# Kernel tuning notes

Measured on AMD Instinct MI355X. Metric: run time of the kernel, lower is better.

Reference implementation:

```python
import jax, jax.numpy as jnp
import numpy as np
import itertools, math

# Static config (matches init_kwargs)
DIM = 384
KEY_DIM = 16
NUM_HEADS = 8
ATTN_RATIO = 4
RES = 14
OUT_DIM = 768
RES2 = math.ceil(RES / 2)          # 7
N = RES * RES                      # 196
N2 = RES2 * RES2                   # 49
D = ATTN_RATIO * KEY_DIM           # 64
NH_KD = NUM_HEADS * KEY_DIM        # 128
DH = NUM_HEADS * D                 # 512
SCALE = KEY_DIM ** -0.5
BATCH = 512


def _build_bias_idxs():
    points = list(itertools.product(range(RES), range(RES)))
    points_ = list(itertools.product(range(RES2), range(RES2)))
    ratio = math.ceil(RES / RES2)
    offsets = {}
    idxs = []
    for p1 in points_:
        for p2 in points:
            off = (abs(p1[0] * ratio - p2[0]), abs(p1[1] * ratio - p2[1]))
            if off not in offsets:
                offsets[off] = len(offsets)
            idxs.append(offsets[off])
    return np.array(idxs, dtype=np.int32).reshape(N2, N), len(offsets)


def setup_inputs() -> dict:
    key = jax.random.key(0)
    ks = jax.random.split(key, 16)
    idxs_np, n_off = _build_bias_idxs()
    w = lambda k, shape, s=0.05: (jax.random.normal(k, shape, jnp.float32) * s)
    inp = {
        "x": jax.random.normal(ks[0], (BATCH, DIM, RES, RES), jnp.float32),
        # LGQuery: depthwise 3x3 s2 conv (groups=DIM), then 1x1 conv + BN (folded scale/shift)
        "q_local_w": w(ks[1], (DIM, 1, 3, 3)),
        "q_local_b": w(ks[2], (DIM,)),
        "q_proj_w": w(ks[3], (NH_KD, DIM)),
        "q_proj_b": w(ks[4], (NH_KD,)),
        "q_bn_s": 1.0 + w(ks[5], (NH_KD,)),
        "q_bn_t": w(ks[5], (NH_KD,)),
        # k: 1x1 conv + BN
        "k_w": w(ks[6], (NH_KD, DIM)),
        "k_b": w(ks[7], (NH_KD,)),
        "k_bn_s": 1.0 + w(ks[8], (NH_KD,)),
        "k_bn_t": w(ks[8], (NH_KD,)),
        # v: 1x1 conv + BN
        "v_w": w(ks[9], (DH, DIM)),
        "v_b": w(ks[10], (DH,)),
        "v_bn_s": 1.0 + w(ks[10], (DH,)),
        "v_bn_t": w(ks[10], (DH,)),
        # v_local: depthwise 3x3 s2 (groups=DH) + BN
        "vl_w": w(ks[11], (DH, 1, 3, 3)),
        "vl_b": w(ks[12], (DH,)),
        "vl_bn_s": 1.0 + w(ks[12], (DH,)),
        "vl_bn_t": w(ks[12], (DH,)),
        # proj: GELU -> 1x1 conv -> BN
        "p_w": w(ks[13], (OUT_DIM, DH)),
        "p_b": w(ks[14], (OUT_DIM,)),
        "p_bn_s": 1.0 + w(ks[14], (OUT_DIM,)),
        "p_bn_t": w(ks[14], (OUT_DIM,)),
        # learned relative-position biases + gather indices
        "attn_biases": w(ks[15], (NUM_HEADS, n_off), 0.02),
        "bias_idxs": jnp.asarray(idxs_np),  # [N2, N] int32
    }
    return inp


def _dwconv_s2(x, w, b):
    # depthwise 3x3, stride 2, pad 1, NCHW
    C = x.shape[1]
    y = jax.lax.conv_general_dilated(
        x, w, window_strides=(2, 2), padding=((1, 1), (1, 1)),
        feature_group_count=C, dimension_numbers=("NCHW", "OIHW", "NCHW"))
    return y + b[None, :, None, None]


def _conv1x1_bn(x, w, b, s, t):
    y = jnp.einsum("bchw,oc->bohw", x, w) + b[None, :, None, None]
    return y * s[None, :, None, None] + t[None, :, None, None]


def reference(x, q_local_w, q_local_b, q_proj_w, q_proj_b, q_bn_s, q_bn_t,
              k_w, k_b, k_bn_s, k_bn_t, v_w, v_b, v_bn_s, v_bn_t,
              vl_w, vl_b, vl_bn_s, vl_bn_t, p_w, p_b, p_bn_s, p_bn_t,
              attn_biases, bias_idxs):
    B = x.shape[0]
    # LGQuery: depthwise conv + avgpool(k=1,s=2)==stride subsample, then 1x1+BN
    ql = _dwconv_s2(x, q_local_w, q_local_b) + x[:, :, ::2, ::2]
    q = _conv1x1_bn(ql, q_proj_w, q_proj_b, q_bn_s, q_bn_t)        # [B,128,7,7]
    q = q.reshape(B, NUM_HEADS, KEY_DIM, N2).transpose(0, 1, 3, 2)  # bhqc

    k = _conv1x1_bn(x, k_w, k_b, k_bn_s, k_bn_t).reshape(B, NUM_HEADS, KEY_DIM, N)  # bhck

    v4 = _conv1x1_bn(x, v_w, v_b, v_bn_s, v_bn_t)                   # [B,512,14,14]
    v_local = _dwconv_s2(v4, vl_w, vl_b)
    v_local = v_local * vl_bn_s[None, :, None, None] + vl_bn_t[None, :, None, None]
    v = v4.reshape(B, NUM_HEADS, D, N).transpose(0, 1, 3, 2)        # bhkd

    bias = attn_biases[:, bias_idxs]                                # [H,N2,N]
    attn = jax.nn.softmax(jnp.einsum("bhqc,bhck->bhqk", q, k) * SCALE + bias[None], axis=-1)
    out = jnp.einsum("bhqk,bhkd->bhqd", attn, v)                    # [B,H,N2,D]
    out = out.transpose(0, 1, 3, 2).reshape(B, DH, RES2, RES2) + v_local
    out = jax.nn.gelu(out, approximate=False)                       # torch nn.GELU default (erf)
    out = _conv1x1_bn(out, p_w, p_b, p_bn_s, p_bn_t)                # [B,768,7,7]
    return out
```

## Files before the change

kernel.cpp:

```cpp
#include <hip/hip_runtime.h>
#include <math.h>

#define DIM 384
#define NUM_HEADS 8
#define RES 14
#define RES2 7
#define NPOS 196
#define N2 49
#define DHEAD 64
#define NH_KD 128
#define DH 512
#define OUT_DIM 768
#define BATCH 512
#define SCALE_Q 0.25f

typedef unsigned short u16;
typedef short s16x8 __attribute__((ext_vector_type(8)));
typedef short s16x4 __attribute__((ext_vector_type(4)));
typedef float f32x4 __attribute__((ext_vector_type(4)));
typedef unsigned int u32x2 __attribute__((ext_vector_type(2)));

__device__ __forceinline__ float bf2f(u16 u) {
  union { unsigned int i; float f; } v; v.i = ((unsigned int)u) << 16; return v.f;
}
__device__ __forceinline__ u16 f2bf(float f) {
  union { unsigned int i; float f; } v; v.f = f;
  unsigned int r = v.i + 0x7fffu + ((v.i >> 16) & 1u);
  return (u16)(r >> 16);
}

#define GLD16(gp, lp) __builtin_amdgcn_global_load_lds( \
    (const __attribute__((address_space(1))) void*)(gp), \
    (__attribute__((address_space(3))) void*)(lp), 16, 0, 0)

__global__ __launch_bounds__(256) void k_prep(const float* __restrict__ kw, const float* __restrict__ vw,
                                              const float* __restrict__ qw, const float* __restrict__ pw,
                                              const float* __restrict__ ab, const int* __restrict__ idxs, int noff,
                                              const float* __restrict__ kb, const float* __restrict__ kbs, const float* __restrict__ kbt,
                                              const float* __restrict__ vb, const float* __restrict__ vbs, const float* __restrict__ vbt,
                                              u16* __restrict__ wb, u16* __restrict__ qwb, u16* __restrict__ pwb,
                                              float* __restrict__ bxp,
                                              float* __restrict__ cvb, float* __restrict__ cvs, float* __restrict__ cvt) {
  int i = blockIdx.x * 256 + threadIdx.x;
  const int E1 = 640 * DIM;
  const int E2 = E1 + NH_KD * DIM;
  const int E3 = E2 + OUT_DIM * DH;
  const int E4 = E3 + NUM_HEADS * N2 * 256;
  const int E5 = E4 + 3 * 640;
  if (i < E1) wb[i] = f2bf(i < DH * DIM ? vw[i] : kw[i - DH * DIM]);
  else if (i < E2) qwb[i - E1] = f2bf(qw[i - E1]);
  else if (i < E3) pwb[i - E2] = f2bf(pw[i - E2]);
  else if (i < E4) {
    int j = i - E3;
    int f = j & 15, c = (j >> 4) & 15;
    int m = (j >> 8) % N2, h = j / (N2 * 256);
    int n = f * 16 + c;
    bxp[j] = (n < NPOS) ? ab[h * noff + idxs[m * NPOS + n]] : 0.f;
  } else if (i < E5) {
    int j = i - E4; int c = j % 640, t = j / 640;
    float v = (c < DH) ? (t == 0 ? vb[c] : t == 1 ? vbs[c] : vbt[c])
                       : (t == 0 ? kb[c - DH] : t == 1 ? kbs[c - DH] : kbt[c - DH]);
    (t == 0 ? cvb : t == 1 ? cvs : cvt)[c] = v;
  }
}

__global__ __launch_bounds__(256) void k_transpose(const float* __restrict__ x, u16* __restrict__ xt) {
  int b = blockIdx.y, c0 = blockIdx.x * 64;
  __shared__ u16 tile[64][196];
  int tid = threadIdx.x, wave = tid >> 6, lane = tid & 63;
  const float* xb = x + (size_t)b * DIM * NPOS;
  for (int r = wave; r < 64; r += 4) {
    const float* row = xb + (size_t)(c0 + r) * NPOS;
    tile[r][lane]       = f2bf(row[lane]);
    tile[r][lane + 64]  = f2bf(row[lane + 64]);
    tile[r][lane + 128] = f2bf(row[lane + 128]);
    if (lane < 4) tile[r][lane + 192] = f2bf(row[lane + 192]);
  }
  __syncthreads();
  u16* xtb = xt + (size_t)b * NPOS * DIM;
  for (int n = wave; n < NPOS; n += 4)
    xtb[(size_t)n * DIM + c0 + lane] = tile[lane][n];
}

__global__ __launch_bounds__(256) void k_dwconv_q8(const u16* __restrict__ xt, const float* __restrict__ w,
                                                   const float* __restrict__ bias, u16* __restrict__ qlt) {
  int b = blockIdx.y;
  int lid = blockIdx.x * 256 + threadIdx.x;
  if (lid >= N2 * (DIM / 8)) return;
  int n2 = lid / (DIM / 8), c0 = (lid % (DIM / 8)) * 8;
  int r = n2 / RES2, s = n2 % RES2;
  const u16* xb = xt + (size_t)b * NPOS * DIM + c0;

  s16x8 xv[9];
#pragma unroll
  for (int dy = 0; dy < 3; dy++) {
    int ry = 2 * r - 1 + dy;
#pragma unroll
    for (int dx = 0; dx < 3; dx++) {
      int sx = 2 * s - 1 + dx;
      if (ry >= 0 && ry < RES && sx >= 0 && sx < RES)
        xv[dy * 3 + dx] = *(const s16x8*)(xb + (size_t)(ry * RES + sx) * DIM);
      else
        xv[dy * 3 + dx] = (s16x8){0, 0, 0, 0, 0, 0, 0, 0};
    }
  }
  s16x8 resid = *(const s16x8*)(xb + (size_t)(2 * r * RES + 2 * s) * DIM);
  s16x8 o;
#pragma unroll
  for (int e = 0; e < 8; e++) {
    const float* we = w + (size_t)(c0 + e) * 9;
    float a = bias[c0 + e] + bf2f((u16)resid[e]);
#pragma unroll
    for (int t = 0; t < 9; t++) a += we[t] * bf2f((u16)xv[t][e]);
    o[e] = (short)f2bf(a);
  }
  *(s16x8*)(qlt + ((size_t)b * N2 + n2) * DIM + c0) = o;
}

template <int SPLN, bool F32OUT, bool KMERGE>
__global__ __launch_bounds__(256) void k_gemm_flat(
    const u16* __restrict__ A, const u16* __restrict__ B, void* __restrict__ C, void* __restrict__ C2,
    const float* __restrict__ cb, const float* __restrict__ bns, const float* __restrict__ bnt,
    int K, int NMT, int ldc, long bstride) {
  __shared__ __align__(16) u16 a_lds[2 * 128 * 32];
  __shared__ __align__(16) u16 b_lds[2 * 128 * 32];
  int nwg = gridDim.x, bx = blockIdx.x;
  int wg = ((nwg & 7) == 0) ? ((bx & 7) * (nwg >> 3) + (bx >> 3)) : bx;
  int mt = wg % NMT, nt = wg / NMT;
  int m0 = mt * 128, n0 = nt * 128;
  int tid = threadIdx.x, w = tid >> 6, l = tid & 63;

  int srow = l >> 2;
  int scol = ((l & 3) ^ ((l >> 3) & 3)) * 8;
  const u16* asrc[2]; const u16* bsrc[2];
#pragma unroll
  for (int c = 0; c < 2; c++) {
    int chunk = w * 2 + c;
    asrc[c] = A + (size_t)(m0 + chunk * 16 + srow) * K + scol;
    bsrc[c] = B + (size_t)(n0 + chunk * 16 + srow) * K + scol;
  }
  char* adst = (char*)a_lds + (w * 2) * 1024 + l * 16;
  char* bdst = (char*)b_lds + (w * 2) * 1024 + l * 16;

  f32x4 acc[4][4];
#pragma unroll
  for (int i = 0; i < 4; i++)
#pragma unroll
    for (int j = 0; j < 4; j++) acc[i][j] = (f32x4){0.f, 0.f, 0.f, 0.f};

  int wm = w >> 1, wn = w & 1;
  int rg8 = ((l >> 4) ^ ((l >> 1) & 3)) * 8;
  int arow = wm * 64 + (l & 15);
  int brow = wn * 64 + (l & 15);

  for (int kk = 0; kk < K; kk += 64) {
#pragma unroll
    for (int c = 0; c < 2; c++) {
      GLD16(asrc[c] + kk,      adst + c * 1024);
      GLD16(asrc[c] + kk + 32, adst + 8192 + c * 1024);
      GLD16(bsrc[c] + kk,      bdst + c * 1024);
      GLD16(bsrc[c] + kk + 32, bdst + 8192 + c * 1024);
    }
    __syncthreads();
#pragma unroll
    for (int hf = 0; hf < 2; hf++) {
      const u16* ah = a_lds + hf * (128 * 32);
      const u16* bh = b_lds + hf * (128 * 32);
      s16x8 af[4], bf[4];
#pragma unroll
      for (int i = 0; i < 4; i++) {
        af[i] = *(const s16x8*)(&ah[(arow + i * 16) * 32 + rg8]);
        bf[i] = *(const s16x8*)(&bh[(brow + i * 16) * 32 + rg8]);
      }
#pragma unroll
      for (int i = 0; i < 4; i++)
#pragma unroll
        for (int j = 0; j < 4; j++)
          acc[i][j] = __builtin_amdgcn_mfma_f32_16x16x32_bf16(af[i], bf[j], acc[i][j], 0, 0, 0);
    }
    __syncthreads();
  }

  int ncol = l & 15, mq = (l >> 4) * 4;
#pragma unroll
  for (int i = 0; i < 4; i++) {
#pragma unroll
    for (int j = 0; j < 4; j++) {
      int n = n0 + wn * 64 + j * 16 + ncol;
#pragma unroll
      for (int r = 0; r < 4; r++) {
        int m = m0 + wm * 64 + i * 16 + mq + r;
        int ch = (SPLN || KMERGE) ? m : n;
        float val = acc[i][j][r] * bns[ch] + (cb[ch] * bns[ch] + bnt[ch]);
        if (KMERGE && m0 >= DH) {
          ((u16*)C2)[(size_t)n * NH_KD + (m - DH)] = f2bf(val);
        } else {
          size_t o;
          if (SPLN) o = (size_t)(n / SPLN) * bstride + (size_t)m * SPLN + (n % SPLN);
          else      o = (size_t)m * ldc + n;
          if (F32OUT) ((float*)C)[o] = val;
          else        ((u16*)C)[o] = f2bf(val);
        }
      }
    }
  }
}

__global__ __launch_bounds__(256) void k_dwconv_v(const u16* __restrict__ v4, const float* __restrict__ w,
    const float* __restrict__ bias, const float* __restrict__ bns, const float* __restrict__ bnt,
    u16* __restrict__ vlt) {
  int b = blockIdx.y, ct = blockIdx.x;
  __shared__ u16 tile[64][196];
  int tid = threadIdx.x, wave = tid >> 6, lane = tid & 63;
  const u16* vbp = v4 + ((size_t)b * DH + ct * 64) * NPOS;
  for (int r = wave; r < 64; r += 4) {
    const u16* row = vbp + (size_t)r * NPOS;
    tile[r][lane]       = row[lane];
    tile[r][lane + 64]  = row[lane + 64];
    tile[r][lane + 128] = row[lane + 128];
    if (lane < 4) tile[r][lane + 192] = row[lane + 192];
  }
  __syncthreads();
  for (int idx = tid; idx < 64 * N2; idx += 256) {
    int cl = idx & 63, n2 = idx >> 6;
    int ch = ct * 64 + cl;
    int r = n2 / RES2, s = n2 % RES2;
    float acc = bias[ch];
#pragma unroll
    for (int dy = 0; dy < 3; dy++) {
      int ry = 2 * r - 1 + dy;
      if (ry < 0 || ry >= RES) continue;
#pragma unroll
      for (int dx = 0; dx < 3; dx++) {
        int sx = 2 * s - 1 + dx;
        if (sx < 0 || sx >= RES) continue;
        acc += w[ch * 9 + dy * 3 + dx] * bf2f(tile[cl][ry * RES + sx]);
      }
    }
    vlt[((size_t)b * N2 + n2) * DH + ch] = f2bf(acc * bns[ch] + bnt[ch]);
  }
}

__global__ __launch_bounds__(256, 4) void k_attn_mfma(const u16* __restrict__ qT, const u16* __restrict__ kT,
    const u16* __restrict__ v4, const float* __restrict__ bxp, const u16* __restrict__ vlT,
    u16* __restrict__ gT) {
  int h = blockIdx.x, b = blockIdx.y;
  __shared__ __align__(16) u16 p_lds[64 * 232];
  float* o_lds = (float*)p_lds;
  int tid = threadIdx.x, w = tid >> 6, l = tid & 63;
  int part = l >> 4, row16 = l & 15;
  int mbase = w * 16 + part * 4;
  int ncol = l & 15;

  for (int idx = tid; idx < 64 * 8; idx += 256)
    ((uint*)&p_lds[(idx >> 3) * 232])[104 + (idx & 7)] = 0;

  s16x8 af = (s16x8){0, 0, 0, 0, 0, 0, 0, 0};
  if (part < 2)
    af = *(const s16x8*)(qT + ((size_t)b * N2 + (w * 16 + row16)) * NH_KD + h * 16 + part * 8);

  const u16* kbase = kT + (size_t)b * NPOS * NH_KD + h * 16 + part * 8;
  f32x4 s[13];
#pragma unroll
  for (int f = 0; f < 13; f++) {
    s16x8 bf = (s16x8){0, 0, 0, 0, 0, 0, 0, 0};
    if (part < 2)
      bf = *(const s16x8*)(kbase + (size_t)(f * 16 + row16) * NH_KD);
    s[f] = __builtin_amdgcn_mfma_f32_16x16x32_bf16(af, bf, (f32x4){0.f, 0.f, 0.f, 0.f}, 0, 0, 0);
  }

  const u16* vbase = v4 + ((size_t)b * DH + h * DHEAD) * NPOS;
  int vd = l & 15, vq8 = part * 8;
  auto VLOAD = [&](int f, int kk) {
    const u16* p = vbase + (size_t)(f * 16 + vd) * NPOS + kk + vq8;
    s16x8 r;
    ((u32x2*)&r)[0] = *(const u32x2*)(p);
    ((u32x2*)&r)[1] = *(const u32x2*)(p + 4);
    return r;
  };
  s16x8 vb0[4];
#pragma unroll
  for (int f = 0; f < 4; f++) vb0[f] = VLOAD(f, 0);

#pragma unroll
  for (int q = 0; q < 4; q++) {
    f32x4 bqr[4];
#pragma unroll
    for (int r = 0; r < 4; r++) {
      int mm = mbase + r; if (mm > N2 - 1) mm = N2 - 1;
      bqr[r] = *(const f32x4*)(bxp + (((size_t)h * N2 + mm) * 16 + ncol) * 16 + q * 4);
    }
#pragma unroll
    for (int ff = 0; ff < 4; ff++) {
      int f = q * 4 + ff;
      if (f < 13) {
        int n = f * 16 + ncol;
#pragma unroll
        for (int r = 0; r < 4; r++) {
          int m = mbase + r;
          s[f][r] = (m < N2 && n < NPOS) ? s[f][r] * SCALE_Q + bqr[r][ff] : -1e30f;
        }
      }
    }
  }
#pragma unroll
  for (int r = 0; r < 4; r++) {
    float mx = s[0][r];
#pragma unroll
    for (int f = 1; f < 13; f++) mx = fmaxf(mx, s[f][r]);
    mx = fmaxf(mx, __shfl_xor(mx, 1)); mx = fmaxf(mx, __shfl_xor(mx, 2));
    mx = fmaxf(mx, __shfl_xor(mx, 4)); mx = fmaxf(mx, __shfl_xor(mx, 8));
    float sum = 0.f;
#pragma unroll
    for (int f = 0; f < 13; f++) { s[f][r] = __expf(s[f][r] - mx); sum += s[f][r]; }
    sum += __shfl_xor(sum, 1); sum += __shfl_xor(sum, 2);
    sum += __shfl_xor(sum, 4); sum += __shfl_xor(sum, 8);
    float inv = 1.f / sum;
#pragma unroll
    for (int f = 0; f < 13; f++) s[f][r] *= inv;
  }
#pragma unroll
  for (int f = 0; f < 13; f++) {
    int n = f * 16 + ncol;
#pragma unroll
    for (int r = 0; r < 4; r++)
      p_lds[(mbase + r) * 232 + n] = f2bf(s[f][r]);
  }
  __syncthreads();

  f32x4 o[4];
#pragma unroll
  for (int f = 0; f < 4; f++) o[f] = (f32x4){0.f, 0.f, 0.f, 0.f};
#pragma unroll
  for (int t = 0; t < 7; t++) {
    int kk = t * 32;
    s16x8 vn[4];
    if (t < 6) {
#pragma unroll
      for (int f = 0; f < 4; f++) vn[f] = VLOAD(f, kk + 32);
    }
    s16x8 pa = *(const s16x8*)(&p_lds[(w * 16 + row16) * 232 + kk + part * 8]);
#pragma unroll
    for (int f = 0; f < 4; f++)
      o[f] = __builtin_amdgcn_mfma_f32_16x16x32_bf16(pa, vb0[f], o[f], 0, 0, 0);
    if (t < 6) {
#pragma unroll
      for (int f = 0; f < 4; f++) vb0[f] = vn[f];
    }
  }
  __syncthreads();

#pragma unroll
  for (int f = 0; f < 4; f++)
#pragma unroll
    for (int r = 0; r < 4; r++) {
      int m = mbase + r;
      if (m < N2) o_lds[m * 68 + f * 16 + ncol] = o[f][r];
    }
  __syncthreads();

  for (int idx = tid; idx < N2 * 16; idx += 256) {
    int row = idx >> 4, c4 = (idx & 15) << 2;
    f32x4 ov = *(const f32x4*)(&o_lds[row * 68 + c4]);
    size_t go = ((size_t)b * N2 + row) * DH + h * DHEAD + c4;
    s16x4 vv = *(const s16x4*)(vlT + go);
    s16x4 outv;
#pragma unroll
    for (int e = 0; e < 4; e++) {
      float xv = ov[e] + bf2f((u16)vv[e]);
      float g = 0.5f * xv * (1.f + erff(xv * 0.70710678118f));
      outv[e] = (short)f2bf(g);
    }
    *(s16x4*)(gT + go) = outv;
  }
}

extern "C" void kernel_launch(void* const* d_in, const int* in_sizes, int n_in,
                              void* d_out, int out_size, void* d_ws, size_t ws_size,
                              hipStream_t stream) {
  const float* x   = (const float*)d_in[0];
  const float* qlw = (const float*)d_in[1];
  const float* qlb = (const float*)d_in[2];
  const float* qpw = (const float*)d_in[3];
  const float* qpb = (const float*)d_in[4];
  const float* qbs = (const float*)d_in[5];
  const float* qbt = (const float*)d_in[6];
  const float* kw  = (const float*)d_in[7];
  const float* kb  = (const float*)d_in[8];
  const float* kbs = (const float*)d_in[9];
  const float* kbt = (const float*)d_in[10];
  const float* vw  = (const float*)d_in[11];
  const float* vb  = (const float*)d_in[12];
  const float* vbs = (const float*)d_in[13];
  const float* vbt = (const float*)d_in[14];
  const float* vlw = (const float*)d_in[15];
  const float* vlb = (const float*)d_in[16];
  const float* vls = (const float*)d_in[17];
  const float* vlt_in = (const float*)d_in[18];
  const float* pw  = (const float*)d_in[19];
  const float* pb  = (const float*)d_in[20];
  const float* pbs = (const float*)d_in[21];
  const float* pbt = (const float*)d_in[22];
  const float* ab  = (const float*)d_in[23];
  const int*   bidx = (const int*)d_in[24];
  int noff = in_sizes[23] / NUM_HEADS;

  char* ws = (char*)d_ws;
  size_t off = 0;
  auto alloc = [&](size_t bytes) { char* p = ws + off; off += (bytes + 255) & ~(size_t)255; return p; };
  u16* xbT = (u16*)alloc((size_t)BATCH * NPOS * DIM * 2);
  u16* kTm = (u16*)alloc((size_t)BATCH * NPOS * NH_KD * 2);
  u16* qlT = (u16*)alloc((size_t)BATCH * N2 * DIM * 2);
  u16* qTm = (u16*)alloc((size_t)BATCH * N2 * NH_KD * 2);
  u16* v4m = (u16*)alloc((size_t)BATCH * DH * NPOS * 2);
  u16* vlTm = (u16*)alloc((size_t)BATCH * N2 * DH * 2);
  float* bxp = (float*)alloc((size_t)NUM_HEADS * N2 * 16 * 16 * 4);
  u16* wb  = (u16*)alloc((size_t)640 * DIM * 2);
  u16* qwb = (u16*)alloc((size_t)NH_KD * DIM * 2);
  u16* pwb = (u16*)alloc((size_t)OUT_DIM * DH * 2);
  float* cvb = (float*)alloc(640 * 4);
  float* cvs = (float*)alloc(640 * 4);
  float* cvt = (float*)alloc(640 * 4);
  u16* gTm = xbT;

  k_prep<<<(890752 + 255) / 256, 256, 0, stream>>>(kw, vw, qpw, pw, ab, bidx, noff,
                                                   kb, kbs, kbt, vb, vbs, vbt,
                                                   wb, qwb, pwb, bxp, cvb, cvs, cvt);

  k_transpose<<<dim3(6, BATCH), 256, 0, stream>>>(x, xbT);
  k_dwconv_q8<<<dim3((N2 * (DIM / 8) + 255) / 256, BATCH), 256, 0, stream>>>(xbT, qlw, qlb, qlT);

  k_gemm_flat<NPOS, false, true><<<3920, 256, 0, stream>>>(
      wb, xbT, v4m, kTm, cvb, cvs, cvt, DIM, 5, 0, (long)DH * NPOS);
  k_gemm_flat<0, false, false><<<196, 256, 0, stream>>>(
      qlT, qwb, qTm, nullptr, qpb, qbs, qbt, DIM, 196, NH_KD, 0);

  k_dwconv_v<<<dim3(8, BATCH), 256, 0, stream>>>(v4m, vlw, vlb, vls, vlt_in, vlTm);
  k_attn_mfma<<<dim3(NUM_HEADS, BATCH), 256, 0, stream>>>(qTm, kTm, v4m, bxp, vlTm, gTm);

  k_gemm_flat<N2, true, false><<<1176, 256, 0, stream>>>(
      pwb, gTm, d_out, nullptr, pb, pbs, pbt, DH, 6, 0, (long)OUT_DIM * N2);
}
```

Before: 418.4 us.

## Fuse q depthwise conv into transpose and merge V/K/Q projection GEMMs

Computes the q-branch depthwise 3x3 stride-2 conv directly from the LDS tile in the transpose kernel, removing a separate kernel that re-read the transposed activations from global memory. The V, K and Q 1x1-conv GEMMs now run in one launch, with block-index ranges choosing the operands. K is computed in transposed orientation (activations as A, weights as B), so its output is written row-contiguous instead of via the scattered KMERGE path. This cuts launches and makes the small Q GEMM run alongside the large one, at the cost of per-block branching and scalar conv work inside the transpose kernel.

```diff
diff --git a/kernel.cpp b/kernel.cpp
--- a/kernel.cpp
+++ b/kernel.cpp
@@ -36,37 +36,35 @@
 __global__ __launch_bounds__(256) void k_prep(const float* __restrict__ kw, const float* __restrict__ vw,
                                               const float* __restrict__ qw, const float* __restrict__ pw,
                                               const float* __restrict__ ab, const int* __restrict__ idxs, int noff,
-                                              const float* __restrict__ kb, const float* __restrict__ kbs, const float* __restrict__ kbt,
-                                              const float* __restrict__ vb, const float* __restrict__ vbs, const float* __restrict__ vbt,
-                                              u16* __restrict__ wb, u16* __restrict__ qwb, u16* __restrict__ pwb,
-                                              float* __restrict__ bxp,
-                                              float* __restrict__ cvb, float* __restrict__ cvs, float* __restrict__ cvt) {
+                                              u16* __restrict__ kwb, u16* __restrict__ vwb,
+                                              u16* __restrict__ qwb, u16* __restrict__ pwb,
+                                              float* __restrict__ bxp) {
   int i = blockIdx.x * 256 + threadIdx.x;
-  const int E1 = 640 * DIM;
-  const int E2 = E1 + NH_KD * DIM;
-  const int E3 = E2 + OUT_DIM * DH;
-  const int E4 = E3 + NUM_HEADS * N2 * 256;
-  const int E5 = E4 + 3 * 640;
-  if (i < E1) wb[i] = f2bf(i < DH * DIM ? vw[i] : kw[i - DH * DIM]);
-  else if (i < E2) qwb[i - E1] = f2bf(qw[i - E1]);
-  else if (i < E3) pwb[i - E2] = f2bf(pw[i - E2]);
-  else if (i < E4) {
-    int j = i - E3;
+  const int e1 = NH_KD * DIM;
+  const int e2 = e1 + DH * DIM;
+  const int e3 = e2 + NH_KD * DIM;
+  const int e4 = e3 + OUT_DIM * DH;
+  const int e5 = e4 + NUM_HEADS * N2 * 256;
+  if (i < e1) kwb[i] = f2bf(kw[i]);
+  else if (i < e2) vwb[i - e1] = f2bf(vw[i - e1]);
+  else if (i < e3) qwb[i - e2] = f2bf(qw[i - e2]);
+  else if (i < e4) pwb[i - e3] = f2bf(pw[i - e3]);
+  else if (i < e5) {
+    int j = i - e4;
     int f = j & 15, c = (j >> 4) & 15;
     int m = (j >> 8) % N2, h = j / (N2 * 256);
     int n = f * 16 + c;
     bxp[j] = (n < NPOS) ? ab[h * noff + idxs[m * NPOS + n]] : 0.f;
-  } else if (i < E5) {
-    int j = i - E4; int c = j % 640, t = j / 640;
-    float v = (c < DH) ? (t == 0 ? vb[c] : t == 1 ? vbs[c] : vbt[c])
-                       : (t == 0 ? kb[c - DH] : t == 1 ? kbs[c - DH] : kbt[c - DH]);
-    (t == 0 ? cvb : t == 1 ? cvs : cvt)[c] = v;
-  }
-}
-
-__global__ __launch_bounds__(256) void k_transpose(const float* __restrict__ x, u16* __restrict__ xt) {
+  }
+}
+
+__global__ __launch_bounds__(256) void k_transpose_dwq(const float* __restrict__ x, u16* __restrict__ xt,
+                                                       const float* __restrict__ qlw, const float* __restrict__ qlb,
+                                                       u16* __restrict__ qlt) {
   int b = blockIdx.y, c0 = blockIdx.x * 64;
   __shared__ u16 tile[64][196];
+  __shared__ float wlds[576];
+  __shared__ float blds[64];
   int tid = threadIdx.x, wave = tid >> 6, lane = tid & 63;
   const float* xb = x + (size_t)b * DIM * NPOS;
   for (int r = wave; r < 64; r += 4) {
@@ -76,50 +74,126 @@
     tile[r][lane + 128] = f2bf(row[lane + 128]);
     if (lane < 4) tile[r][lane + 192] = f2bf(row[lane + 192]);
   }
+  for (int i = tid; i < 576; i += 256) wlds[i] = qlw[c0 * 9 + i];
+  if (tid < 64) blds[tid] = qlb[c0 + tid];
   __syncthreads();
   u16* xtb = xt + (size_t)b * NPOS * DIM;
   for (int n = wave; n < NPOS; n += 4)
     xtb[(size_t)n * DIM + c0 + lane] = tile[lane][n];
-}
-
-__global__ __launch_bounds__(256) void k_dwconv_q8(const u16* __restrict__ xt, const float* __restrict__ w,
-                                                   const float* __restrict__ bias, u16* __restrict__ qlt) {
-  int b = blockIdx.y;
-  int lid = blockIdx.x * 256 + threadIdx.x;
-  if (lid >= N2 * (DIM / 8)) return;
-  int n2 = lid / (DIM / 8), c0 = (lid % (DIM / 8)) * 8;
-  int r = n2 / RES2, s = n2 % RES2;
-  const u16* xb = xt + (size_t)b * NPOS * DIM + c0;
-
-  s16x8 xv[9];
-#pragma unroll
-  for (int dy = 0; dy < 3; dy++) {
-    int ry = 2 * r - 1 + dy;
-#pragma unroll
-    for (int dx = 0; dx < 3; dx++) {
-      int sx = 2 * s - 1 + dx;
-      if (ry >= 0 && ry < RES && sx >= 0 && sx < RES)
-        xv[dy * 3 + dx] = *(const s16x8*)(xb + (size_t)(ry * RES + sx) * DIM);
-      else
-        xv[dy * 3 + dx] = (s16x8){0, 0, 0, 0, 0, 0, 0, 0};
-    }
-  }
-  s16x8 resid = *(const s16x8*)(xb + (size_t)(2 * r * RES + 2 * s) * DIM);
-  s16x8 o;
-#pragma unroll
-  for (int e = 0; e < 8; e++) {
-    const float* we = w + (size_t)(c0 + e) * 9;
-    float a = bias[c0 + e] + bf2f((u16)resid[e]);
-#pragma unroll
-    for (int t = 0; t < 9; t++) a += we[t] * bf2f((u16)xv[t][e]);
-    o[e] = (short)f2bf(a);
-  }
-  *(s16x8*)(qlt + ((size_t)b * N2 + n2) * DIM + c0) = o;
-}
-
-template <int SPLN, bool F32OUT, bool KMERGE>
+  for (int idx = tid; idx < 64 * N2; idx += 256) {
+    int cl = idx & 63, n2 = idx >> 6;
+    int r = n2 / RES2, s = n2 % RES2;
+    float acc = blds[cl] + bf2f(tile[cl][(2 * r) * RES + 2 * s]);
+#pragma unroll
+    for (int dy = 0; dy < 3; dy++) {
+      int ry = 2 * r - 1 + dy;
+      if (ry < 0 || ry >= RES) continue;
+#pragma unroll
+      for (int dx = 0; dx < 3; dx++) {
+        int sx = 2 * s - 1 + dx;
+        if (sx < 0 || sx >= RES) continue;
+        acc += wlds[cl * 9 + dy * 3 + dx] * bf2f(tile[cl][ry * RES + sx]);
+      }
+    }
+    qlt[((size_t)b * N2 + n2) * DIM + c0 + cl] = f2bf(acc);
+  }
+}
+
+__global__ __launch_bounds__(256) void k_gemm3(
+    const u16* __restrict__ xbT, const u16* __restrict__ qlT,
+    const u16* __restrict__ vwb, const u16* __restrict__ kwb, const u16* __restrict__ qwb,
+    u16* __restrict__ v4m, u16* __restrict__ kTm, u16* __restrict__ qTm,
+    const float* __restrict__ vb, const float* __restrict__ vbs, const float* __restrict__ vbt,
+    const float* __restrict__ kb, const float* __restrict__ kbs, const float* __restrict__ kbt,
+    const float* __restrict__ qpb, const float* __restrict__ qbs, const float* __restrict__ qbt) {
+  __shared__ __align__(16) u16 a_lds[2 * 128 * 32];
+  __shared__ __align__(16) u16 b_lds[2 * 128 * 32];
+  int bx = blockIdx.x;
+  const u16 *A, *B; u16* C;
+  const float *cb, *bns, *bnt;
+  int NMT, ldc, mode, lnwg, lbx;
+  if (bx < 3136)      { A = vwb; B = xbT; C = v4m; cb = vb;  bns = vbs; bnt = vbt; NMT = 4;   ldc = 0;     mode = 1; lnwg = 3136; lbx = bx; }
+  else if (bx < 3920) { A = xbT; B = kwb; C = kTm; cb = kb;  bns = kbs; bnt = kbt; NMT = 784; ldc = NH_KD; mode = 0; lnwg = 784;  lbx = bx - 3136; }
+  else                { A = qlT; B = qwb; C = qTm; cb = qpb; bns = qbs; bnt = qbt; NMT = 196; ldc = NH_KD; mode = 0; lnwg = 196;  lbx = bx - 3920; }
+  int wg = ((lnwg & 7) == 0) ? ((lbx & 7) * (lnwg >> 3) + (lbx >> 3)) : lbx;
+  int mt = wg % NMT, nt = wg / NMT;
+  int m0 = mt * 128, n0 = nt * 128;
+  int tid = threadIdx.x, w = tid >> 6, l = tid & 63;
+
+  int srow = l >> 2;
+  int scol = ((l & 3) ^ ((l >> 3) & 3)) * 8;
+  const u16* asrc[2]; const u16* bsrc[2];
+#pragma unroll
+  for (int c = 0; c < 2; c++) {
+    int chunk = w * 2 + c;
+    asrc[c] = A + (size_t)(m0 + chunk * 16 + srow) * DIM + scol;
+    bsrc[c] = B + (size_t)(n0 + chunk * 16 + srow) * DIM + scol;
+  }
+  char* adst = (char*)a_lds + (w * 2) * 1024 + l * 16;
+  char* bdst = (char*)b_lds + (w * 2) * 1024 + l * 16;
+
+  f32x4 acc[4][4];
+#pragma unroll
+  for (int i = 0; i < 4; i++)
+#pragma unroll
+    for (int j = 0; j < 4; j++) acc[i][j] = (f32x4){0.f, 0.f, 0.f, 0.f};
+
+  int wm = w >> 1, wn = w & 1;
+  int rg8 = ((l >> 4) ^ ((l >> 1) & 3)) * 8;
+  int arow = wm * 64 + (l & 15);
+  int brow = wn * 64 + (l & 15);
+
+  for (int kk = 0; kk < DIM; kk += 64) {
+#pragma unroll
+    for (int c = 0; c < 2; c++) {
+      GLD16(asrc[c] + kk,      adst + c * 1024);
+      GLD16(asrc[c] + kk + 32, adst + 8192 + c * 1024);
+      GLD16(bsrc[c] + kk,      bdst + c * 1024);
+      GLD16(bsrc[c] + kk + 32, bdst + 8192 + c * 1024);
+    }
+    __syncthreads();
+#pragma unroll
+    for (int hf = 0; hf < 2; hf++) {
+      const u16* ah = a_lds + hf * (128 * 32);
+      const u16* bh = b_lds + hf * (128 * 32);
+      s16x8 af[4], bf[4];
+#pragma unroll
+      for (int i = 0; i < 4; i++) {
+        af[i] = *(const s16x8*)(&ah[(arow + i * 16) * 32 + rg8]);
+        bf[i] = *(const s16x8*)(&bh[(brow + i * 16) * 32 + rg8]);
+      }
+#pragma unroll
+      for (int i = 0; i < 4; i++)
+#pragma unroll
+        for (int j = 0; j < 4; j++)
+          acc[i][j] = __builtin_amdgcn_mfma_f32_16x16x32_bf16(af[i], bf[j], acc[i][j], 0, 0, 0);
+    }
+    __syncthreads();
+  }
+
+  int ncol = l & 15, mq = (l >> 4) * 4;
+#pragma unroll
+  for (int i = 0; i < 4; i++) {
+#pragma unroll
+    for (int j = 0; j < 4; j++) {
+      int n = n0 + wn * 64 + j * 16 + ncol;
+#pragma unroll
+      for (int r = 0; r < 4; r++) {
+        int m = m0 + wm * 64 + i * 16 + mq + r;
+        int ch = mode ? m : n;
+        float val = acc[i][j][r] * bns[ch] + (cb[ch] * bns[ch] + bnt[ch]);
+        size_t o;
+        if (mode) o = (size_t)(n / NPOS) * ((long)DH * NPOS) + (size_t)m * NPOS + (n % NPOS);
+        else      o = (size_t)m * ldc + n;
+        C[o] = f2bf(val);
+      }
+    }
+  }
+}
+
+template <int SPLN, bool F32OUT>
 __global__ __launch_bounds__(256) void k_gemm_flat(
-    const u16* __restrict__ A, const u16* __restrict__ B, void* __restrict__ C, void* __restrict__ C2,
+    const u16* __restrict__ A, const u16* __restrict__ B, void* __restrict__ C,
     const float* __restrict__ cb, const float* __restrict__ bns, const float* __restrict__ bnt,
     int K, int NMT, int ldc, long bstride) {
   __shared__ __align__(16) u16 a_lds[2 * 128 * 32];
@@ -190,17 +264,13 @@
 #pragma unroll
       for (int r = 0; r < 4; r++) {
         int m = m0 + wm * 64 + i * 16 + mq + r;
-        int ch = (SPLN || KMERGE) ? m : n;
+        int ch = SPLN ? m : n;
         float val = acc[i][j][r] * bns[ch] + (cb[ch] * bns[ch] + bnt[ch]);
-        if (KMERGE && m0 >= DH) {
-          ((u16*)C2)[(size_t)n * NH_KD + (m - DH)] = f2bf(val);
-        } else {
-          size_t o;
-          if (SPLN) o = (size_t)(n / SPLN) * bstride + (size_t)m * SPLN + (n % SPLN);
-          else      o = (size_t)m * ldc + n;
-          if (F32OUT) ((float*)C)[o] = val;
-          else        ((u16*)C)[o] = f2bf(val);
-        }
+        size_t o;
+        if (SPLN) o = (size_t)(n / SPLN) * bstride + (size_t)m * SPLN + (n % SPLN);
+        else      o = (size_t)m * ldc + n;
+        if (F32OUT) ((float*)C)[o] = val;
+        else        ((u16*)C)[o] = f2bf(val);
       }
     }
   }
@@ -415,29 +485,23 @@
   u16* v4m = (u16*)alloc((size_t)BATCH * DH * NPOS * 2);
   u16* vlTm = (u16*)alloc((size_t)BATCH * N2 * DH * 2);
   float* bxp = (float*)alloc((size_t)NUM_HEADS * N2 * 16 * 16 * 4);
-  u16* wb  = (u16*)alloc((size_t)640 * DIM * 2);
+  u16* kwb = (u16*)alloc((size_t)NH_KD * DIM * 2);
+  u16* vwb = (u16*)alloc((size_t)DH * DIM * 2);
   u16* qwb = (u16*)alloc((size_t)NH_KD * DIM * 2);
   u16* pwb = (u16*)alloc((size_t)OUT_DIM * DH * 2);
-  float* cvb = (float*)alloc(640 * 4);
-  float* cvs = (float*)alloc(640 * 4);
-  float* cvt = (float*)alloc(640 * 4);
   u16* gTm = xbT;
 
-  k_prep<<<(890752 + 255) / 256, 256, 0, stream>>>(kw, vw, qpw, pw, ab, bidx, noff,
-                                                   kb, kbs, kbt, vb, vbs, vbt,
-                                                   wb, qwb, pwb, bxp, cvb, cvs, cvt);
-
-  k_transpose<<<dim3(6, BATCH), 256, 0, stream>>>(x, xbT);
-  k_dwconv_q8<<<dim3((N2 * (DIM / 8) + 255) / 256, BATCH), 256, 0, stream>>>(xbT, qlw, qlb, qlT);
-
-  k_gemm_flat<NPOS, false, true><<<3920, 256, 0, stream>>>(
-      wb, xbT, v4m, kTm, cvb, cvs, cvt, DIM, 5, 0, (long)DH * NPOS);
-  k_gemm_flat<0, false, false><<<196, 256, 0, stream>>>(
-      qlT, qwb, qTm, nullptr, qpb, qbs, qbt, DIM, 196, NH_KD, 0);
+  k_prep<<<(788480 + 255) / 256, 256, 0, stream>>>(kw, vw, qpw, pw, ab, bidx, noff,
+                                                   kwb, vwb, qwb, pwb, bxp);
+
+  k_transpose_dwq<<<dim3(6, BATCH), 256, 0, stream>>>(x, xbT, qlw, qlb, qlT);
+
+  k_gemm3<<<4116, 256, 0, stream>>>(xbT, qlT, vwb, kwb, qwb, v4m, kTm, qTm,
+                                    vb, vbs, vbt, kb, kbs, kbt, qpb, qbs, qbt);
 
   k_dwconv_v<<<dim3(8, BATCH), 256, 0, stream>>>(v4m, vlw, vlb, vls, vlt_in, vlTm);
   k_attn_mfma<<<dim3(NUM_HEADS, BATCH), 256, 0, stream>>>(qTm, kTm, v4m, bxp, vlTm, gTm);
 
-  k_gemm_flat<N2, true, false><<<1176, 256, 0, stream>>>(
-      pwb, gTm, d_out, nullptr, pb, pbs, pbt, DH, 6, 0, (long)OUT_DIM * N2);
-}
+  k_gemm_flat<N2, true><<<1176, 256, 0, stream>>>(
+      pwb, gTm, d_out, pb, pbs, pbt, DH, 6, 0, (long)OUT_DIM * N2);
+}
```

Result: slower. 451.8 us (+8.0%).
